# Performance work log

Measured on AMD Instinct MI355X. Metric: run time of the kernel, lower is better.

## Reference

```python
import jax, jax.numpy as jnp
import numpy as np

B, T, F, UNITS = 256, 256, 64, 512


def _lstm(x, W, Uw, b):
    """Keras-style LSTM with activation=relu, recurrent_activation=sigmoid.
    x: [B,T,F_in]; W: [F_in,4U]; Uw: [U,4U]; b: [4U]. Gate order i,f,c,o.
    Returns (all_h [B,T,U], last_h [B,U])."""
    n = Uw.shape[0]
    xg = jnp.einsum('btf,fg->btg', x, W) + b  # precompute input projections [B,T,4U]

    def step(carry, xg_t):
        h, c = carry
        z = xg_t + h @ Uw  # [B,4U]
        i, f, g, o = jnp.split(z, 4, axis=-1)
        i = jax.nn.sigmoid(i)
        f = jax.nn.sigmoid(f)
        g = jax.nn.relu(g)          # candidate activation = relu
        o = jax.nn.sigmoid(o)
        c = f * c + i * g
        h = o * jax.nn.relu(c)      # output activation = relu
        return (h, c), h

    h0 = jnp.zeros((x.shape[0], n), x.dtype)
    (hT, _), hs = jax.lax.scan(step, (h0, jnp.zeros_like(h0)), jnp.swapaxes(xg, 0, 1))
    return jnp.swapaxes(hs, 0, 1), hT


def setup_inputs() -> dict:
    key = jax.random.key(0)
    ks = jax.random.split(key, 8)
    s = 0.05
    return {
        'x':  jax.random.normal(ks[0], (B, T, F), jnp.float32),
        'W1': jax.random.normal(ks[1], (F, 4 * UNITS), jnp.float32) * s,
        'U1': jax.random.normal(ks[2], (UNITS, 4 * UNITS), jnp.float32) * s,
        'b1': jnp.zeros((4 * UNITS,), jnp.float32),
        'W2': jax.random.normal(ks[3], (UNITS, 4 * UNITS), jnp.float32) * s,
        'U2': jax.random.normal(ks[4], (UNITS, 4 * UNITS), jnp.float32) * s,
        'b2': jnp.zeros((4 * UNITS,), jnp.float32),
        'Wd': jax.random.normal(ks[5], (UNITS, 1), jnp.float32) * s,
        'bd': jnp.zeros((1,), jnp.float32),
    }


def reference(x, W1, U1, b1, W2, U2, b2, Wd, bd):
    h1, _ = _lstm(x, W1, U1, b1)      # return_sequences=True; dropout identity at inference
    _, h2 = _lstm(h1, W2, U2, b2)     # return_sequences=False -> last hidden state
    return jax.nn.sigmoid(h2 @ Wd + bd)  # [B,1]
```

## Files before the change

kernel.cpp:

```cpp
#include <hip/hip_runtime.h>
#include <hip/hip_bf16.h>

#define B_  256
#define T_  256
#define F_  64
#define U_  512
#define NG_ 2048
#define BU_ (B_ * U_)

typedef __attribute__((ext_vector_type(8))) short short8;
typedef __attribute__((ext_vector_type(16))) float floatx16;

__device__ __forceinline__ unsigned short f2bf(float f) {
    union { float f; unsigned int u; } v; v.f = f;
    unsigned int u = v.u;
    return (unsigned short)((u + 0x7FFFu + ((u >> 16) & 1u)) >> 16);
}
__device__ __forceinline__ float bf2f(unsigned short s) {
    union { unsigned int u; float f; } v; v.u = ((unsigned int)s) << 16;
    return v.f;
}

__global__ void cast_x_kernel(const float* __restrict__ x,
                              unsigned short* __restrict__ xb, int n) {
    int i = blockIdx.x * blockDim.x + threadIdx.x;
    if (i < n) xb[i] = f2bf(x[i]);
}

__global__ void pack32_kernel(const float* __restrict__ W, const float* __restrict__ Uw,
                              unsigned short* __restrict__ dst, int KT, int KX) {
    long tid = (long)blockIdx.x * blockDim.x + threadIdx.x;
    long total = 16L * 4 * KT * 512;
    if (tid >= total) return;
    int j    = (int)(tid & 7);
    int lane = (int)((tid >> 3) & 63);
    int p512 = (int)(tid >> 9);
    int kt   = p512 % KT;
    int q    = (p512 / KT) & 3;
    int ug   = p512 / (KT * 4);
    int srcn = q * U_ + ug * 32 + (lane & 31);
    int k    = kt * 16 + (lane >> 5) * 8 + j;
    float v  = (k < KX) ? W[(long)k * NG_ + srcn] : Uw[(long)(k - KX) * NG_ + srcn];
    dst[tid] = f2bf(v);
}

__device__ __forceinline__ short8 llc_load(const unsigned short* p) {
    short8 r;
    asm volatile("global_load_dwordx4 %0, %1, off sc0 sc1" : "=v"(r) : "v"(p));
    return r;
}
#define VMWAIT(N) asm volatile("s_waitcnt vmcnt(" #N ")" ::: "memory")
__device__ __forceinline__ void dep8(short8& x) { asm volatile("" : "+v"(x)); }

#define MFMA32(a, b, c) __builtin_amdgcn_mfma_f32_32x32x16_bf16(a, b, c, 0, 0, 0)

__device__ __forceinline__ void wait_dual(const int* fa, int ta,
                                          const int* fb, int tb, int lane) {
    const int* p  = (lane < 32) ? (fa + (lane & 15) * 32) : (fb + (lane & 15) * 32);
    const int tgt = (lane < 32) ? ta : tb;
    int guard = 0;
    for (;;) {
        int v = __hip_atomic_load(p, __ATOMIC_RELAXED, __HIP_MEMORY_SCOPE_AGENT);
        if (__ballot(v >= tgt) == ~0ull) break;
        __builtin_amdgcn_s_sleep(1);
        if (++guard > (1 << 19)) break;
    }
}

__global__ __launch_bounds__(512, 1) void lstm_persist(
    const unsigned short* __restrict__ xb,
    const unsigned short* __restrict__ P1,
    const unsigned short* __restrict__ P2,
    const float* __restrict__ b1, const float* __restrict__ b2,
    unsigned short* __restrict__ h1r, unsigned short* __restrict__ h2r,
    int* flagsA, int* flagsB)
{
    const int bid  = blockIdx.x;
    const bool isL1 = (bid < 128);
    const int sub  = isL1 ? bid : (bid - 128);
    const int mo   = sub & 7;
    const int ug   = sub >> 3;
    const int tid  = threadIdx.x;
    const int w    = tid >> 6;
    const int lane = tid & 63;
    const int arow = lane & 31;
    const int koff = (lane >> 5) * 8;
    const int row  = mo * 32 + arow;

    int* fA_ = flagsA + mo * 16 * 32;
    int* fB_ = flagsB + mo * 16 * 32;

    __shared__ float red[8][4][32][33];
    __shared__ float cst[32][32];
    __shared__ float bias_s[4][32];

    for (int i = tid; i < 1024; i += 512) cst[i >> 5][i & 31] = 0.f;
    if (tid < 128) {
        const float* bb = isL1 ? b1 : b2;
        bias_s[tid >> 5][tid & 31] = bb[(tid >> 5) * U_ + ug * 32 + (tid & 31)];
    }

    if (isL1) {
        const int kbase = (w < 4) ? w * 5 : 20 + (w - 4) * 4;
        const int kcnt  = (w < 4) ? 5 : 4;
        short8 wf[4][5];
        {
            const unsigned short* base = P1 + (size_t)ug * (4 * 36 * 512);
            #pragma unroll
            for (int q = 0; q < 4; ++q) {
                #pragma unroll
                for (int i = 0; i < 5; ++i) {
                    if (i < kcnt)
                        wf[q][i] = *(const short8*)(base
                            + ((size_t)(q * 36 + kbase + i) * 64 + lane) * 8);
                }
            }
        }
        __syncthreads();

        for (int k = 0; k < T_; ++k) {
            floatx16 acc[4];
            #pragma unroll
            for (int q = 0; q < 4; ++q) {
                #pragma unroll
                for (int i = 0; i < 16; ++i) acc[q][i] = 0.f;
            }

            if (w == 0) {
                const unsigned short* xbase = xb + ((size_t)row * T_ + k) * F_;
                #pragma unroll
                for (int g = 0; g < 4; ++g) {
                    short8 a = *(const short8*)(xbase + g * 16 + koff);
                    #pragma unroll
                    for (int q = 0; q < 4; ++q) acc[q] = MFMA32(a, wf[q][g], acc[q]);
                }
            } else if (w == 7) {
                if (k >= 1) wait_dual(fA_, k, fB_, k - 3, lane);
            }
            __syncthreads();
            __atomic_signal_fence(__ATOMIC_ACQUIRE);

            if (k >= 1) {
                if (w == 0) {
                    const unsigned short* hb = h1r + (size_t)((k - 1) & 3) * BU_
                                               + (size_t)row * U_;
                    short8 fa0 = llc_load(hb + koff);
                    VMWAIT(0);
                    dep8(fa0);
                    #pragma unroll
                    for (int q = 0; q < 4; ++q) acc[q] = MFMA32(fa0, wf[q][4], acc[q]);
                } else {
                    const unsigned short* hb = h1r + (size_t)((k - 1) & 3) * BU_
                                               + (size_t)row * U_ + (kbase - 4) * 16;
                    short8 fa[5];
                    #pragma unroll
                    for (int i = 0; i < 5; ++i)
                        if (i < kcnt) fa[i] = llc_load(hb + i * 16 + koff);
                    VMWAIT(0);
                    #pragma unroll
                    for (int i = 0; i < 5; ++i) {
                        if (i < kcnt) {
                            dep8(fa[i]);
                            #pragma unroll
                            for (int q = 0; q < 4; ++q)
                                acc[q] = MFMA32(fa[i], wf[q][i], acc[q]);
                        }
                    }
                }
            }

            #pragma unroll
            for (int r = 0; r < 16; ++r) {
                int rr = (r & 3) + 8 * (r >> 2) + 4 * (lane >> 5);
                #pragma unroll
                for (int q = 0; q < 4; ++q) red[w][q][rr][arow] = acc[q][r];
            }
            __syncthreads();

            {
                int r = tid >> 4, u2 = (tid & 15) * 2;
                unsigned int pk = 0;
                #pragma unroll
                for (int du = 0; du < 2; ++du) {
                    int u = u2 + du;
                    float zi = 0.f, zf = 0.f, zg = 0.f, zo = 0.f;
                    #pragma unroll
                    for (int ww = 0; ww < 8; ++ww) {
                        zi += red[ww][0][r][u];
                        zf += red[ww][1][r][u];
                        zg += red[ww][2][r][u];
                        zo += red[ww][3][r][u];
                    }
                    zi += bias_s[0][u]; zf += bias_s[1][u];
                    zg += bias_s[2][u]; zo += bias_s[3][u];
                    float si = 1.f / (1.f + __expf(-zi));
                    float sf = 1.f / (1.f + __expf(-zf));
                    float so = 1.f / (1.f + __expf(-zo));
                    float gg = zg > 0.f ? zg : 0.f;
                    float cn = sf * cst[r][u] + si * gg;
                    cst[r][u] = cn;
                    float hn = so * (cn > 0.f ? cn : 0.f);
                    pk |= ((unsigned int)f2bf(hn)) << (16 * du);
                }
                unsigned int* hp = (unsigned int*)(h1r + (size_t)(k & 3) * BU_
                                   + (size_t)(mo * 32 + (tid >> 4)) * U_ + ug * 32 + u2);
                __hip_atomic_store(hp, pk, __ATOMIC_RELAXED, __HIP_MEMORY_SCOPE_AGENT);
            }
            __syncthreads();
            __atomic_signal_fence(__ATOMIC_RELEASE);
            if (tid == 0)
                __hip_atomic_store(fA_ + ug * 32, k + 1, __ATOMIC_RELAXED,
                                   __HIP_MEMORY_SCOPE_AGENT);
        }
    } else {
        short8 wf[4][8];
        {
            const unsigned short* base = P2 + (size_t)ug * (4 * 64 * 512);
            #pragma unroll
            for (int q = 0; q < 4; ++q) {
                #pragma unroll
                for (int i = 0; i < 8; ++i)
                    wf[q][i] = *(const short8*)(base
                        + ((size_t)(q * 64 + w * 8 + i) * 64 + lane) * 8);
            }
        }
        __syncthreads();

        for (int t = 0; t < T_; ++t) {
            if (w == 7) wait_dual(fA_, t + 1, fB_, t, lane);
            __syncthreads();
            __atomic_signal_fence(__ATOMIC_ACQUIRE);

            floatx16 acc[4];
            #pragma unroll
            for (int q = 0; q < 4; ++q) {
                #pragma unroll
                for (int i = 0; i < 16; ++i) acc[q][i] = 0.f;
            }

            const bool isU2 = (w >= 4);
            if (!isU2 || t >= 1) {
                const unsigned short* hb = isU2
                    ? h2r + (size_t)((t - 1) & 3) * BU_ + (size_t)row * U_ + (w - 4) * 128
                    : h1r + (size_t)(t & 3) * BU_       + (size_t)row * U_ + w * 128;
                short8 fb[8];
                #pragma unroll
                for (int i = 0; i < 8; ++i) fb[i] = llc_load(hb + i * 16 + koff);
                VMWAIT(0);
                #pragma unroll
                for (int i = 0; i < 8; ++i) {
                    dep8(fb[i]);
                    #pragma unroll
                    for (int q = 0; q < 4; ++q) acc[q] = MFMA32(fb[i], wf[q][i], acc[q]);
                }
            }

            #pragma unroll
            for (int r = 0; r < 16; ++r) {
                int rr = (r & 3) + 8 * (r >> 2) + 4 * (lane >> 5);
                #pragma unroll
                for (int q = 0; q < 4; ++q) red[w][q][rr][arow] = acc[q][r];
            }
            __syncthreads();

            {
                int r = tid >> 4, u2 = (tid & 15) * 2;
                unsigned int pk = 0;
                #pragma unroll
                for (int du = 0; du < 2; ++du) {
                    int u = u2 + du;
                    float zi = 0.f, zf = 0.f, zg = 0.f, zo = 0.f;
                    #pragma unroll
                    for (int ww = 0; ww < 8; ++ww) {
                        zi += red[ww][0][r][u];
                        zf += red[ww][1][r][u];
                        zg += red[ww][2][r][u];
                        zo += red[ww][3][r][u];
                    }
                    zi += bias_s[0][u]; zf += bias_s[1][u];
                    zg += bias_s[2][u]; zo += bias_s[3][u];
                    float si = 1.f / (1.f + __expf(-zi));
                    float sf = 1.f / (1.f + __expf(-zf));
                    float so = 1.f / (1.f + __expf(-zo));
                    float gg = zg > 0.f ? zg : 0.f;
                    float cn = sf * cst[r][u] + si * gg;
                    cst[r][u] = cn;
                    float hn = so * (cn > 0.f ? cn : 0.f);
                    pk |= ((unsigned int)f2bf(hn)) << (16 * du);
                }
                unsigned int* hp = (unsigned int*)(h2r + (size_t)(t & 3) * BU_
                                   + (size_t)(mo * 32 + (tid >> 4)) * U_ + ug * 32 + u2);
                __hip_atomic_store(hp, pk, __ATOMIC_RELAXED, __HIP_MEMORY_SCOPE_AGENT);
            }
            __syncthreads();
            __atomic_signal_fence(__ATOMIC_RELEASE);
            if (tid == 0)
                __hip_atomic_store(fB_ + ug * 32, t + 1, __ATOMIC_RELAXED,
                                   __HIP_MEMORY_SCOPE_AGENT);
        }
    }
}

__global__ void dense_kernel(const unsigned short* __restrict__ h2,
                             const float* __restrict__ Wd,
                             const float* __restrict__ bd,
                             float* __restrict__ out) {
    int b = blockIdx.x;
    int lane = threadIdx.x;
    const unsigned short* hp = h2 + (long)b * U_ + lane * 8;
    float sum = 0.f;
    #pragma unroll
    for (int j = 0; j < 8; ++j) sum += bf2f(hp[j]) * Wd[lane * 8 + j];
    #pragma unroll
    for (int off = 32; off; off >>= 1) sum += __shfl_down(sum, off);
    if (lane == 0) out[b] = 1.f / (1.f + __expf(-(sum + bd[0])));
}

extern "C" void kernel_launch(void* const* d_in, const int* in_sizes, int n_in,
                              void* d_out, int out_size, void* d_ws, size_t ws_size,
                              hipStream_t stream) {
    const float* x  = (const float*)d_in[0];
    const float* W1 = (const float*)d_in[1];
    const float* U1 = (const float*)d_in[2];
    const float* b1 = (const float*)d_in[3];
    const float* W2 = (const float*)d_in[4];
    const float* U2 = (const float*)d_in[5];
    const float* b2 = (const float*)d_in[6];
    const float* Wd = (const float*)d_in[7];
    const float* bd = (const float*)d_in[8];
    float* out = (float*)d_out;

    char* ws = (char*)d_ws;
    size_t off = 0;
    unsigned short* xb  = (unsigned short*)(ws + off); off += (size_t)B_ * T_ * F_ * 2;
    unsigned short* P1  = (unsigned short*)(ws + off); off += (size_t)16 * 4 * 36 * 512 * 2;
    unsigned short* P2  = (unsigned short*)(ws + off); off += (size_t)16 * 4 * 64 * 512 * 2;
    unsigned short* h1r = (unsigned short*)(ws + off); off += (size_t)4 * BU_ * 2;
    unsigned short* h2r = (unsigned short*)(ws + off); off += (size_t)4 * BU_ * 2;
    int* flagsA = (int*)(ws + off); off += (size_t)8 * 16 * 32 * 4;
    int* flagsB = (int*)(ws + off); off += (size_t)8 * 16 * 32 * 4;

    (void)hipMemsetAsync(flagsA, 0, (size_t)8 * 16 * 32 * 4 * 2, stream);

    int n = B_ * T_ * F_;
    cast_x_kernel<<<(n + 255) / 256, 256, 0, stream>>>(x, xb, n);
    {
        long tot1 = 16L * 4 * 36 * 512;
        pack32_kernel<<<(int)((tot1 + 255) / 256), 256, 0, stream>>>(W1, U1, P1, 36, 64);
        long tot2 = 16L * 4 * 64 * 512;
        pack32_kernel<<<(int)((tot2 + 255) / 256), 256, 0, stream>>>(W2, U2, P2, 64, 512);
    }

    lstm_persist<<<256, 512, 0, stream>>>(xb, P1, P2, b1, b2, h1r, h2r,
                                          flagsA, flagsB);

    dense_kernel<<<B_, 64, 0, stream>>>(h2r + (size_t)((T_ - 1) & 3) * BU_,
                                        Wd, bd, out);
}
```

Measured before the change: 1.282 ms.

## Replace flag-based inter-block sync with sentinel-polled full history buffers

```diff
diff --git a/kernel.cpp b/kernel.cpp
--- a/kernel.cpp
+++ b/kernel.cpp
@@ -49,21 +49,40 @@
     asm volatile("global_load_dwordx4 %0, %1, off sc0 sc1" : "=v"(r) : "v"(p));
     return r;
 }
+__device__ __forceinline__ void sys_store_u32(unsigned int* p, unsigned int v) {
+    asm volatile("global_store_dword %0, %1, off sc0 sc1" :: "v"(p), "v"(v) : "memory");
+}
 #define VMWAIT(N) asm volatile("s_waitcnt vmcnt(" #N ")" ::: "memory")
 __device__ __forceinline__ void dep8(short8& x) { asm volatile("" : "+v"(x)); }
 
 #define MFMA32(a, b, c) __builtin_amdgcn_mfma_f32_32x32x16_bf16(a, b, c, 0, 0, 0)
 
-__device__ __forceinline__ void wait_dual(const int* fa, int ta,
-                                          const int* fb, int tb, int lane) {
-    const int* p  = (lane < 32) ? (fa + (lane & 15) * 32) : (fb + (lane & 15) * 32);
-    const int tgt = (lane < 32) ? ta : tb;
-    int guard = 0;
+__device__ __forceinline__ void lds_barrier() {
+    __builtin_amdgcn_sched_barrier(0);
+    asm volatile("s_waitcnt lgkmcnt(0)" ::: "memory");
+    __builtin_amdgcn_s_barrier();
+    __builtin_amdgcn_sched_barrier(0);
+}
+
+template<int N, int M>
+__device__ __forceinline__ void wait_fresh(short8 (&d)[M], const unsigned short* b, int koff) {
+    int g = 0;
     for (;;) {
-        int v = __hip_atomic_load(p, __ATOMIC_RELAXED, __HIP_MEMORY_SCOPE_AGENT);
-        if (__ballot(v >= tgt) == ~0ull) break;
-        __builtin_amdgcn_s_sleep(1);
-        if (++guard > (1 << 19)) break;
+        VMWAIT(0);
+        __builtin_amdgcn_sched_barrier(0);
+        #pragma unroll
+        for (int i = 0; i < N; ++i) dep8(d[i]);
+        bool bad = false;
+        #pragma unroll
+        for (int i = 0; i < N; ++i) {
+            union { short8 s; unsigned int w[4]; } u; u.s = d[i];
+            #pragma unroll
+            for (int j = 0; j < 4; ++j) bad |= (u.w[j] == 0xFFFFFFFFu);
+        }
+        if (__ballot(bad) == 0ull) break;
+        if (++g > (1 << 15)) break;
+        #pragma unroll
+        for (int i = 0; i < N; ++i) d[i] = llc_load(b + i * 16 + koff);
     }
 }
 
@@ -72,8 +91,7 @@
     const unsigned short* __restrict__ P1,
     const unsigned short* __restrict__ P2,
     const float* __restrict__ b1, const float* __restrict__ b2,
-    unsigned short* __restrict__ h1r, unsigned short* __restrict__ h2r,
-    int* flagsA, int* flagsB)
+    unsigned short* __restrict__ h1h, unsigned short* __restrict__ h2h)
 {
     const int bid  = blockIdx.x;
     const bool isL1 = (bid < 128);
@@ -87,9 +105,6 @@
     const int koff = (lane >> 5) * 8;
     const int row  = mo * 32 + arow;
 
-    int* fA_ = flagsA + mo * 16 * 32;
-    int* fB_ = flagsB + mo * 16 * 32;
-
     __shared__ float red[8][4][32][33];
     __shared__ float cst[32][32];
     __shared__ float bias_s[4][32];
@@ -134,37 +149,43 @@
                     #pragma unroll
                     for (int q = 0; q < 4; ++q) acc[q] = MFMA32(a, wf[q][g], acc[q]);
                 }
-            } else if (w == 7) {
-                if (k >= 1) wait_dual(fA_, k, fB_, k - 3, lane);
-            }
-            __syncthreads();
-            __atomic_signal_fence(__ATOMIC_ACQUIRE);
+            }
 
             if (k >= 1) {
                 if (w == 0) {
-                    const unsigned short* hb = h1r + (size_t)((k - 1) & 3) * BU_
+                    const unsigned short* hb = h1h + (size_t)(k - 1) * BU_
                                                + (size_t)row * U_;
-                    short8 fa0 = llc_load(hb + koff);
-                    VMWAIT(0);
-                    dep8(fa0);
-                    #pragma unroll
-                    for (int q = 0; q < 4; ++q) acc[q] = MFMA32(fa0, wf[q][4], acc[q]);
-                } else {
-                    const unsigned short* hb = h1r + (size_t)((k - 1) & 3) * BU_
+                    short8 fa[1];
+                    fa[0] = llc_load(hb + koff);
+                    wait_fresh<1>(fa, hb, koff);
+                    dep8(fa[0]);
+                    #pragma unroll
+                    for (int q = 0; q < 4; ++q) acc[q] = MFMA32(fa[0], wf[q][4], acc[q]);
+                } else if (w < 4) {
+                    const unsigned short* hb = h1h + (size_t)(k - 1) * BU_
                                                + (size_t)row * U_ + (kbase - 4) * 16;
                     short8 fa[5];
                     #pragma unroll
-                    for (int i = 0; i < 5; ++i)
-                        if (i < kcnt) fa[i] = llc_load(hb + i * 16 + koff);
-                    VMWAIT(0);
+                    for (int i = 0; i < 5; ++i) fa[i] = llc_load(hb + i * 16 + koff);
+                    wait_fresh<5>(fa, hb, koff);
                     #pragma unroll
                     for (int i = 0; i < 5; ++i) {
-                        if (i < kcnt) {
-                            dep8(fa[i]);
-                            #pragma unroll
-                            for (int q = 0; q < 4; ++q)
-                                acc[q] = MFMA32(fa[i], wf[q][i], acc[q]);
-                        }
+                        dep8(fa[i]);
+                        #pragma unroll
+                        for (int q = 0; q < 4; ++q) acc[q] = MFMA32(fa[i], wf[q][i], acc[q]);
+                    }
+                } else {
+                    const unsigned short* hb = h1h + (size_t)(k - 1) * BU_
+                                               + (size_t)row * U_ + (kbase - 4) * 16;
+                    short8 fa[4];
+                    #pragma unroll
+                    for (int i = 0; i < 4; ++i) fa[i] = llc_load(hb + i * 16 + koff);
+                    wait_fresh<4>(fa, hb, koff);
+                    #pragma unroll
+                    for (int i = 0; i < 4; ++i) {
+                        dep8(fa[i]);
+                        #pragma unroll
+                        for (int q = 0; q < 4; ++q) acc[q] = MFMA32(fa[i], wf[q][i], acc[q]);
                     }
                 }
             }
@@ -175,7 +196,7 @@
                 #pragma unroll
                 for (int q = 0; q < 4; ++q) red[w][q][rr][arow] = acc[q][r];
             }
-            __syncthreads();
+            lds_barrier();
 
             {
                 int r = tid >> 4, u2 = (tid & 15) * 2;
@@ -202,15 +223,11 @@
                     float hn = so * (cn > 0.f ? cn : 0.f);
                     pk |= ((unsigned int)f2bf(hn)) << (16 * du);
                 }
-                unsigned int* hp = (unsigned int*)(h1r + (size_t)(k & 3) * BU_
-                                   + (size_t)(mo * 32 + (tid >> 4)) * U_ + ug * 32 + u2);
-                __hip_atomic_store(hp, pk, __ATOMIC_RELAXED, __HIP_MEMORY_SCOPE_AGENT);
-            }
-            __syncthreads();
-            __atomic_signal_fence(__ATOMIC_RELEASE);
-            if (tid == 0)
-                __hip_atomic_store(fA_ + ug * 32, k + 1, __ATOMIC_RELAXED,
-                                   __HIP_MEMORY_SCOPE_AGENT);
+                unsigned int* hp = (unsigned int*)(h1h + (size_t)k * BU_
+                                   + (size_t)(mo * 32 + r) * U_ + ug * 32 + u2);
+                sys_store_u32(hp, pk);
+            }
+            lds_barrier();
         }
     } else {
         short8 wf[4][8];
@@ -227,10 +244,6 @@
         __syncthreads();
 
         for (int t = 0; t < T_; ++t) {
-            if (w == 7) wait_dual(fA_, t + 1, fB_, t, lane);
-            __syncthreads();
-            __atomic_signal_fence(__ATOMIC_ACQUIRE);
-
             floatx16 acc[4];
             #pragma unroll
             for (int q = 0; q < 4; ++q) {
@@ -241,12 +254,12 @@
             const bool isU2 = (w >= 4);
             if (!isU2 || t >= 1) {
                 const unsigned short* hb = isU2
-                    ? h2r + (size_t)((t - 1) & 3) * BU_ + (size_t)row * U_ + (w - 4) * 128
-                    : h1r + (size_t)(t & 3) * BU_       + (size_t)row * U_ + w * 128;
+                    ? h2h + (size_t)(t - 1) * BU_ + (size_t)row * U_ + (w - 4) * 128
+                    : h1h + (size_t)t * BU_       + (size_t)row * U_ + w * 128;
                 short8 fb[8];
                 #pragma unroll
                 for (int i = 0; i < 8; ++i) fb[i] = llc_load(hb + i * 16 + koff);
-                VMWAIT(0);
+                wait_fresh<8>(fb, hb, koff);
                 #pragma unroll
                 for (int i = 0; i < 8; ++i) {
                     dep8(fb[i]);
@@ -261,7 +274,7 @@
                 #pragma unroll
                 for (int q = 0; q < 4; ++q) red[w][q][rr][arow] = acc[q][r];
             }
-            __syncthreads();
+            lds_barrier();
 
             {
                 int r = tid >> 4, u2 = (tid & 15) * 2;
@@ -288,15 +301,11 @@
                     float hn = so * (cn > 0.f ? cn : 0.f);
                     pk |= ((unsigned int)f2bf(hn)) << (16 * du);
                 }
-                unsigned int* hp = (unsigned int*)(h2r + (size_t)(t & 3) * BU_
-                                   + (size_t)(mo * 32 + (tid >> 4)) * U_ + ug * 32 + u2);
-                __hip_atomic_store(hp, pk, __ATOMIC_RELAXED, __HIP_MEMORY_SCOPE_AGENT);
-            }
-            __syncthreads();
-            __atomic_signal_fence(__ATOMIC_RELEASE);
-            if (tid == 0)
-                __hip_atomic_store(fB_ + ug * 32, t + 1, __ATOMIC_RELAXED,
-                                   __HIP_MEMORY_SCOPE_AGENT);
+                unsigned int* hp = (unsigned int*)(h2h + (size_t)t * BU_
+                                   + (size_t)(mo * 32 + r) * U_ + ug * 32 + u2);
+                sys_store_u32(hp, pk);
+            }
+            lds_barrier();
         }
     }
 }
@@ -335,12 +344,10 @@
     unsigned short* xb  = (unsigned short*)(ws + off); off += (size_t)B_ * T_ * F_ * 2;
     unsigned short* P1  = (unsigned short*)(ws + off); off += (size_t)16 * 4 * 36 * 512 * 2;
     unsigned short* P2  = (unsigned short*)(ws + off); off += (size_t)16 * 4 * 64 * 512 * 2;
-    unsigned short* h1r = (unsigned short*)(ws + off); off += (size_t)4 * BU_ * 2;
-    unsigned short* h2r = (unsigned short*)(ws + off); off += (size_t)4 * BU_ * 2;
-    int* flagsA = (int*)(ws + off); off += (size_t)8 * 16 * 32 * 4;
-    int* flagsB = (int*)(ws + off); off += (size_t)8 * 16 * 32 * 4;
-
-    (void)hipMemsetAsync(flagsA, 0, (size_t)8 * 16 * 32 * 4 * 2, stream);
+    unsigned short* h1h = (unsigned short*)(ws + off); off += (size_t)T_ * BU_ * 2;
+    unsigned short* h2h = (unsigned short*)(ws + off); off += (size_t)T_ * BU_ * 2;
+
+    (void)hipMemsetAsync(h1h, 0xFF, (size_t)2 * T_ * BU_ * 2, stream);
 
     int n = B_ * T_ * F_;
     cast_x_kernel<<<(n + 255) / 256, 256, 0, stream>>>(x, xb, n);
@@ -351,9 +358,8 @@
         pack32_kernel<<<(int)((tot2 + 255) / 256), 256, 0, stream>>>(W2, U2, P2, 64, 512);
     }
 
-    lstm_persist<<<256, 512, 0, stream>>>(xb, P1, P2, b1, b2, h1r, h2r,
-                                          flagsA, flagsB);
-
-    dense_kernel<<<B_, 64, 0, stream>>>(h2r + (size_t)((T_ - 1) & 3) * BU_,
+    lstm_persist<<<256, 512, 0, stream>>>(xb, P1, P2, b1, b2, h1h, h2h);
+
+    dense_kernel<<<B_, 64, 0, stream>>>(h2h + (size_t)(T_ - 1) * BU_,
                                         Wd, bd, out);
 }
```

Result: faster. 1.187 ms (-7.4%).
